# Performance work log

Hardware: AMD Instinct MI355X
Metric: run time of the kernel (lower is better)

Reference implementation:

```python
import jax, jax.numpy as jnp
import numpy as np

N = 100000
E = 1600000
IN = 256
H = 4
C = 64


def setup_inputs() -> dict:
    key = jax.random.key(0)
    k1, k2, k3, k4, k5, k6 = jax.random.split(key, 6)
    x = jax.random.normal(k1, (N, IN), dtype=jnp.float32)
    edge_index = jax.random.randint(k2, (2, E), 0, N, dtype=jnp.int64)
    W = jax.random.normal(k3, (IN, H * C), dtype=jnp.float32) * (1.0 / np.sqrt(IN))
    att_src = jax.random.normal(k4, (H, C), dtype=jnp.float32) * 0.1
    att_dst = jax.random.normal(k5, (H, C), dtype=jnp.float32) * 0.1
    bias = jax.random.normal(k6, (H * C,), dtype=jnp.float32) * 0.01
    return {"x": x, "edge_index": edge_index, "W": W, "att_src": att_src, "att_dst": att_dst, "bias": bias}


def reference(x, edge_index, W, att_src, att_dst, bias):
    n = x.shape[0]
    # PyG GATConv default: add self-loops
    loops = jnp.arange(n, dtype=edge_index.dtype)
    src = jnp.concatenate([edge_index[0], loops])  # [E+N]
    dst = jnp.concatenate([edge_index[1], loops])  # [E+N]
    xp = (x @ W).reshape(n, H, C)                   # [N,H,C]
    a_src = jnp.einsum('nhc,hc->nh', xp, att_src)   # [N,H]
    a_dst = jnp.einsum('nhc,hc->nh', xp, att_dst)   # [N,H]
    # per-edge attention logits, LeakyReLU(0.2)
    alpha = jax.nn.leaky_relu(a_src[src] + a_dst[dst], negative_slope=0.2)  # [E+N,H]
    # segment softmax over destination neighborhoods (every node has a self-loop)
    amax = jax.ops.segment_max(alpha, dst, num_segments=n)
    amax = jnp.where(jnp.isfinite(amax), amax, 0.0)
    ex = jnp.exp(alpha - amax[dst])
    denom = jax.ops.segment_sum(ex, dst, num_segments=n)
    w = ex / denom[dst]                              # [E+N,H]
    # weighted scatter-add of source features
    msg = xp[src] * w[..., None]                     # [E+N,H,C]
    agg = jax.ops.segment_sum(msg, dst, num_segments=n)  # [N,H,C]
    out = agg.reshape(n, H * C) + bias
    return jax.nn.elu(out)
```

## Files before the change

kernel.cpp:

```cpp
#include <hip/hip_runtime.h>
#include <hip/hip_fp16.h>

#define FDIM 256
#define NH 4

typedef float f32x4 __attribute__((ext_vector_type(4)));
typedef int   i32x4 __attribute__((ext_vector_type(4)));
typedef short short8v __attribute__((ext_vector_type(8)));
typedef unsigned short ushort_t;
typedef unsigned short ushort8 __attribute__((ext_vector_type(8)));

__device__ __forceinline__ float leaky02(float v) { return v > 0.0f ? v : 0.2f * v; }

__device__ __forceinline__ ushort_t f2bf(float f) {
    union { float f; unsigned int u; } v; v.f = f;
    unsigned int u = v.u + 0x7FFFu + ((v.u >> 16) & 1u);
    return (ushort_t)(u >> 16);
}

__device__ __forceinline__ float bf2f(ushort_t u) {
    union { float f; unsigned int u; } v;
    v.u = ((unsigned int)u) << 16;
    return v.f;
}

__device__ __forceinline__ void gload_lds16(const void* g, void* lds) {
    __builtin_amdgcn_global_load_lds((const __attribute__((address_space(1))) unsigned int*)g,
                                     (__attribute__((address_space(3))) unsigned int*)lds, 16, 0, 0);
}

__device__ __forceinline__ float recw(const i32x4& r, int h) {
    unsigned v = (h < 2) ? (unsigned)r.y : (unsigned)r.z;
    unsigned bits = (h & 1) ? (v >> 16) : (v & 0xFFFFu);
    __half_raw hr; hr.x = (unsigned short)bits;
    return __half2float(*reinterpret_cast<__half*>(&hr));
}

__global__ __launch_bounds__(256) void wprep_kernel(const float* __restrict__ W,
                                                    ushort_t* __restrict__ Wbf) {
    const int k = blockIdx.x;
    const int col = threadIdx.x;
    Wbf[(((size_t)(k >> 3) * 256 + col) << 3) + (k & 7)] = f2bf(W[(size_t)k * 256 + col]);
}

__global__ __launch_bounds__(512) void gemm_xp_kernel(const float* __restrict__ x,
                                                      const ushort_t* __restrict__ Wbf,
                                                      const float* __restrict__ att_s,
                                                      const float* __restrict__ att_d,
                                                      ushort_t* __restrict__ xpb,
                                                      float* __restrict__ a_src,
                                                      float* __restrict__ a_dst, int n,
                                                      const int* __restrict__ dst,
                                                      int* __restrict__ counts,
                                                      ushort_t* __restrict__ rank, int E) {
    __shared__ ushort_t a_lds[4096];
    __shared__ ushort_t b_lds[8192];
    const int t = threadIdx.x;

    const int w = t >> 6, l = t & 63;
    const int wm = w >> 2, wn = w & 3;
    const int row0 = blockIdx.x << 7;
    const int fr = l & 15, fk = l >> 4;

    const int arow = t & 127, akb = t >> 7;
    int grow = row0 + arow;
    if (grow >= n) grow = n - 1;
    const float* aptr = x + (size_t)grow * FDIM + (akb << 3);

    f32x4 acc[4][4] = {};

    for (int s = 0; s < 8; ++s) {
        float4 v0 = *(const float4*)(aptr + s * 32);
        float4 v1 = *(const float4*)(aptr + s * 32 + 4);
        ushort8 u;
        u[0]=f2bf(v0.x); u[1]=f2bf(v0.y); u[2]=f2bf(v0.z); u[3]=f2bf(v0.w);
        u[4]=f2bf(v1.x); u[5]=f2bf(v1.y); u[6]=f2bf(v1.z); u[7]=f2bf(v1.w);

        if (s) __syncthreads();

        *(ushort8*)&a_lds[(((size_t)akb << 7) + arow) << 3] = u;
        gload_lds16(Wbf + (size_t)s * 8192 + ((size_t)t << 3), (char*)b_lds + (w << 10));
        gload_lds16(Wbf + (size_t)s * 8192 + ((size_t)(t + 512) << 3), (char*)b_lds + 8192 + (w << 10));
        __syncthreads();

        short8v af[4], bfv[4];
        #pragma unroll
        for (int m = 0; m < 4; ++m)
            af[m] = *(const short8v*)&a_lds[(((size_t)fk << 7) + wm * 64 + m * 16 + fr) << 3];
        #pragma unroll
        for (int nf = 0; nf < 4; ++nf)
            bfv[nf] = *(const short8v*)&b_lds[(((size_t)fk << 8) + wn * 64 + nf * 16 + fr) << 3];
        #pragma unroll
        for (int m = 0; m < 4; ++m)
            #pragma unroll
            for (int nf = 0; nf < 4; ++nf)
                acc[m][nf] = __builtin_amdgcn_mfma_f32_16x16x32_bf16(af[m], bfv[nf], acc[m][nf], 0, 0, 0);
    }

    #pragma unroll
    for (int m = 0; m < 4; ++m) {
        const int r_ = row0 + wm * 64 + m * 16 + fk * 4;
        #pragma unroll
        for (int nf = 0; nf < 4; ++nf) {
            const int c_ = wn * 64 + nf * 16 + fr;
            #pragma unroll
            for (int j = 0; j < 4; ++j)
                if (r_ + j < n)
                    xpb[(size_t)(r_ + j) * FDIM + c_] = f2bf(acc[m][nf][j]);
        }
    }

    float att_sv[4], att_dv[4];
    #pragma unroll
    for (int nf = 0; nf < 4; ++nf) {
        att_sv[nf] = att_s[(wn << 6) + (nf << 4) + fr];
        att_dv[nf] = att_d[(wn << 6) + (nf << 4) + fr];
    }
    #pragma unroll
    for (int m = 0; m < 4; ++m) {
        #pragma unroll
        for (int j = 0; j < 4; ++j) {
            float ps = acc[m][0][j] * att_sv[0] + acc[m][1][j] * att_sv[1]
                     + acc[m][2][j] * att_sv[2] + acc[m][3][j] * att_sv[3];
            float pd = acc[m][0][j] * att_dv[0] + acc[m][1][j] * att_dv[1]
                     + acc[m][2][j] * att_dv[2] + acc[m][3][j] * att_dv[3];
            ps += __shfl_xor(ps, 1, 64); pd += __shfl_xor(pd, 1, 64);
            ps += __shfl_xor(ps, 2, 64); pd += __shfl_xor(pd, 2, 64);
            ps += __shfl_xor(ps, 4, 64); pd += __shfl_xor(pd, 4, 64);
            ps += __shfl_xor(ps, 8, 64); pd += __shfl_xor(pd, 8, 64);
            if (fr == 0) {
                const int r_ = row0 + wm * 64 + m * 16 + fk * 4 + j;
                if (r_ < n) {
                    a_src[r_ * NH + wn] = ps;
                    a_dst[r_ * NH + wn] = pd;
                }
            }
        }
    }

    {
        const int per = (E + gridDim.x - 1) / gridDim.x;
        const int lo = blockIdx.x * per;
        const int hi = min(lo + per, E);
        for (int e = lo + t; e < hi; e += 512) {
            const int d = __builtin_nontemporal_load(&dst[e]);
            rank[e] = (ushort_t)atomicAdd(&counts[d], 1);
        }
    }
}

__global__ __launch_bounds__(256) void scan_partial_kernel(const int* __restrict__ counts,
                                                           int* __restrict__ blockSums, int n) {
    __shared__ int sdata[256];
    const int b = blockIdx.x, t = threadIdx.x;
    const int base = b * 1024 + t * 4;
    int s = 0;
    #pragma unroll
    for (int j = 0; j < 4; ++j)
        if (base + j < n) s += counts[base + j];
    sdata[t] = s;
    __syncthreads();
    for (int off = 128; off > 0; off >>= 1) {
        if (t < off) sdata[t] += sdata[t + off];
        __syncthreads();
    }
    if (t == 0) blockSums[b] = sdata[0];
}

__global__ __launch_bounds__(256) void scan_final_kernel(const int* __restrict__ counts,
                                                         const int* __restrict__ blockSums,
                                                         int* __restrict__ offsets, int n, int nb) {
    __shared__ int s[256];
    __shared__ int bs[256];
    const int b = blockIdx.x, t = threadIdx.x;
    int bv = (t < nb) ? blockSums[t] : 0;
    bs[t] = bv;
    __syncthreads();
    for (int d = 1; d < 256; d <<= 1) {
        int u = (t >= d) ? bs[t - d] : 0;
        __syncthreads();
        bs[t] += u;
        __syncthreads();
    }
    const int blockOff = (b > 0) ? bs[b - 1] : 0;

    const int base = b * 1024 + t * 4;
    int c[4];
    int tsum = 0;
    #pragma unroll
    for (int j = 0; j < 4; ++j) {
        c[j] = (base + j < n) ? counts[base + j] : 0;
        tsum += c[j];
    }
    s[t] = tsum;
    __syncthreads();
    for (int d = 1; d < 256; d <<= 1) {
        int u = (t >= d) ? s[t - d] : 0;
        __syncthreads();
        s[t] += u;
        __syncthreads();
    }
    int run = s[t] - tsum + blockOff;
    #pragma unroll
    for (int j = 0; j < 4; ++j) {
        if (base + j < n) {
            offsets[base + j] = run;
            run += c[j];
        }
    }
}

__global__ void scatter_kernel(const int* __restrict__ src, const int* __restrict__ dst,
                               const ushort_t* __restrict__ rank,
                               const float* __restrict__ a_src, const float* __restrict__ a_dst,
                               const int* __restrict__ offsets,
                               i32x4* __restrict__ erec, int E) {
    int stride = gridDim.x * blockDim.x;
    for (int e = blockIdx.x * blockDim.x + threadIdx.x; e < E; e += stride) {
        const int s = __builtin_nontemporal_load(&src[e]);
        const int d = __builtin_nontemporal_load(&dst[e]);
        const int r = rank[e];
        const float4 as = ((const float4*)a_src)[s];
        const float4 ad = ((const float4*)a_dst)[d];
        const float w0 = __expf(leaky02(as.x + ad.x));
        const float w1 = __expf(leaky02(as.y + ad.y));
        const float w2 = __expf(leaky02(as.z + ad.z));
        const float w3 = __expf(leaky02(as.w + ad.w));
        union { __half2 h; int i; } p01, p23;
        p01.h = __floats2half2_rn(w0, w1);
        p23.h = __floats2half2_rn(w2, w3);
        i32x4 rec;
        rec.x = s; rec.y = p01.i; rec.z = p23.i; rec.w = 0;
        const int pos = offsets[d] + r;
        __builtin_nontemporal_store(rec, &erec[pos]);
    }
}

__global__ __launch_bounds__(256) void aggregate_kernel(const ushort_t* __restrict__ xpb,
                                                        const float* __restrict__ a_src,
                                                        const float* __restrict__ a_dst,
                                                        const int* __restrict__ offsets,
                                                        const int* __restrict__ counts,
                                                        const i32x4* __restrict__ erec,
                                                        const float* __restrict__ bias,
                                                        float* __restrict__ out, int n) {
    const int i = (blockIdx.x << 2) + (threadIdx.x >> 6);
    if (i >= n) return;
    const int lane = threadIdx.x & 63;
    const int halfid = lane >> 5, sl = lane & 31;
    const int h = sl >> 3;
    const size_t colb = (size_t)sl << 3;
    const int start = offsets[i];
    const int cnt = counts[i];
    const i32x4* recs = erec + start;

    float acc[8] = {};
    float den = 0.f;

    int e = 0;
    for (; e + 4 <= cnt; e += 4) {
        const i32x4 ra = recs[e + halfid];
        const i32x4 rb = recs[e + 2 + halfid];
        const ushort8 ua = *(const ushort8*)(xpb + (size_t)ra.x * FDIM + colb);
        const ushort8 ub = *(const ushort8*)(xpb + (size_t)rb.x * FDIM + colb);
        const float wa = recw(ra, h), wb = recw(rb, h);
        den += wa + wb;
        #pragma unroll
        for (int j = 0; j < 8; ++j) acc[j] = fmaf(wa, bf2f(ua[j]), acc[j]);
        #pragma unroll
        for (int j = 0; j < 8; ++j) acc[j] = fmaf(wb, bf2f(ub[j]), acc[j]);
    }
    for (; e < cnt; e += 2) {
        const int idx = e + halfid;
        const int cidx = idx < cnt ? idx : cnt - 1;
        const i32x4 r = recs[cidx];
        const ushort8 u = *(const ushort8*)(xpb + (size_t)r.x * FDIM + colb);
        const float wv = idx < cnt ? recw(r, h) : 0.f;
        den += wv;
        #pragma unroll
        for (int j = 0; j < 8; ++j) acc[j] = fmaf(wv, bf2f(u[j]), acc[j]);
    }
    if (halfid == 0) {
        const float ws = __expf(leaky02(a_src[i * NH + h] + a_dst[i * NH + h]));
        const ushort8 u = *(const ushort8*)(xpb + (size_t)i * FDIM + colb);
        den += ws;
        #pragma unroll
        for (int j = 0; j < 8; ++j) acc[j] = fmaf(ws, bf2f(u[j]), acc[j]);
    }
    den += __shfl_xor(den, 32, 64);
    #pragma unroll
    for (int j = 0; j < 8; ++j) acc[j] += __shfl_xor(acc[j], 32, 64);

    const float inv = 1.0f / den;
    const int c0 = (sl << 3) + (halfid << 2);
    const float4 b4 = *(const float4*)(bias + c0);
    const int jb = halfid << 2;
    f32x4 v;
    v.x = acc[jb + 0] * inv + b4.x;
    v.y = acc[jb + 1] * inv + b4.y;
    v.z = acc[jb + 2] * inv + b4.z;
    v.w = acc[jb + 3] * inv + b4.w;
    v.x = v.x > 0.f ? v.x : (__expf(v.x) - 1.f);
    v.y = v.y > 0.f ? v.y : (__expf(v.y) - 1.f);
    v.z = v.z > 0.f ? v.z : (__expf(v.z) - 1.f);
    v.w = v.w > 0.f ? v.w : (__expf(v.w) - 1.f);
    *(f32x4*)(out + (size_t)i * FDIM + c0) = v;
}

extern "C" void kernel_launch(void* const* d_in, const int* in_sizes, int n_in,
                              void* d_out, int out_size, void* d_ws, size_t ws_size,
                              hipStream_t stream) {
    const float* x       = (const float*)d_in[0];
    const int*   ei      = (const int*)d_in[1];
    const float* W       = (const float*)d_in[2];
    const float* att_s   = (const float*)d_in[3];
    const float* att_d   = (const float*)d_in[4];
    const float* bias    = (const float*)d_in[5];
    float* out = (float*)d_out;

    const int n = in_sizes[0] / FDIM;
    const int E = in_sizes[1] / 2;
    const int* src = ei;
    const int* dst = ei + E;

    char* ws = (char*)d_ws;
    size_t off = 0;
    auto alloc = [&](size_t bytes) -> void* {
        void* p = ws + off;
        off = (off + bytes + 255) & ~(size_t)255;
        return p;
    };
    ushort_t* xpb  = (ushort_t*)alloc((size_t)n * FDIM * sizeof(ushort_t));
    float* a_src   = (float*)alloc((size_t)n * NH * sizeof(float));
    float* a_dst   = (float*)alloc((size_t)n * NH * sizeof(float));
    int* counts    = (int*)alloc((size_t)n * sizeof(int));
    int* offsets   = (int*)alloc((size_t)n * sizeof(int));
    int* blockSums = (int*)alloc(256 * sizeof(int));
    ushort_t* rank = (ushort_t*)alloc((size_t)E * sizeof(ushort_t));
    i32x4* erec    = (i32x4*)alloc((size_t)E * sizeof(i32x4));
    ushort_t* Wbf  = (ushort_t*)alloc((size_t)FDIM * FDIM * sizeof(ushort_t));
    (void)ws_size;

    hipMemsetAsync(counts, 0, (size_t)n * sizeof(int), stream);

    wprep_kernel<<<256, 256, 0, stream>>>(W, Wbf);
    gemm_xp_kernel<<<(n + 127) / 128, 512, 0, stream>>>(x, Wbf, att_s, att_d, xpb, a_src, a_dst, n,
                                                        dst, counts, rank, E);
    const int nb = (n + 1023) / 1024;
    scan_partial_kernel<<<nb, 256, 0, stream>>>(counts, blockSums, n);
    scan_final_kernel<<<nb, 256, 0, stream>>>(counts, blockSums, offsets, n, nb);
    scatter_kernel<<<2048, 256, 0, stream>>>(src, dst, rank, a_src, a_dst, offsets, erec, E);
    aggregate_kernel<<<(n + 3) / 4, 256, 0, stream>>>(xpb, a_src, a_dst, offsets, counts, erec,
                                                      bias, out, n);
}
```

Baseline: 334.3 us.

## Pre-convert x to bf16 in separate kernel and load GEMM tiles via global_load_lds

Moves the fp32-to-bf16 conversion of x and the edge rank counting into a new prep kernel that writes a bf16 copy of x. The GEMM then streams both A and B tiles directly into LDS with global_load_lds instead of loading fp32 through registers, converting, and storing to LDS. This is meant to shorten the GEMM's per-stage latency and decouple the atomic counting from it. The cost is an extra full write and read of a 51 MB bf16 copy of x plus one more kernel launch.

New measurement: 332.1 us. Within noise of the previous version (-0.7%).

```diff
diff --git a/kernel.cpp b/kernel.cpp
--- a/kernel.cpp
+++ b/kernel.cpp
@@ -43,44 +43,70 @@
     Wbf[(((size_t)(k >> 3) * 256 + col) << 3) + (k & 7)] = f2bf(W[(size_t)k * 256 + col]);
 }
 
-__global__ __launch_bounds__(512) void gemm_xp_kernel(const float* __restrict__ x,
+__global__ __launch_bounds__(256) void xprep_kernel(const float* __restrict__ x,
+                                                    ushort_t* __restrict__ xb, int n,
+                                                    const int* __restrict__ dst,
+                                                    int* __restrict__ counts,
+                                                    ushort_t* __restrict__ rank, int E) {
+    const int stride = gridDim.x * blockDim.x;
+    const int gid = blockIdx.x * blockDim.x + threadIdx.x;
+    const int total8 = n * 32;
+    for (int idx = gid; idx < total8; idx += stride) {
+        const float4 v0 = ((const float4*)x)[(size_t)idx * 2];
+        const float4 v1 = ((const float4*)x)[(size_t)idx * 2 + 1];
+        ushort8 u;
+        u[0]=f2bf(v0.x); u[1]=f2bf(v0.y); u[2]=f2bf(v0.z); u[3]=f2bf(v0.w);
+        u[4]=f2bf(v1.x); u[5]=f2bf(v1.y); u[6]=f2bf(v1.z); u[7]=f2bf(v1.w);
+        *(ushort8*)(xb + (size_t)idx * 8) = u;
+    }
+    for (int e = gid; e < E; e += stride) {
+        const int d = __builtin_nontemporal_load(&dst[e]);
+        rank[e] = (ushort_t)atomicAdd(&counts[d], 1);
+    }
+}
+
+__global__ __launch_bounds__(512) void gemm_xp_kernel(const ushort_t* __restrict__ xb,
                                                       const ushort_t* __restrict__ Wbf,
                                                       const float* __restrict__ att_s,
                                                       const float* __restrict__ att_d,
                                                       ushort_t* __restrict__ xpb,
                                                       float* __restrict__ a_src,
-                                                      float* __restrict__ a_dst, int n,
-                                                      const int* __restrict__ dst,
-                                                      int* __restrict__ counts,
-                                                      ushort_t* __restrict__ rank, int E) {
+                                                      float* __restrict__ a_dst, int n) {
     __shared__ ushort_t a_lds[4096];
     __shared__ ushort_t b_lds[8192];
     const int t = threadIdx.x;
-
     const int w = t >> 6, l = t & 63;
     const int wm = w >> 2, wn = w & 3;
     const int row0 = blockIdx.x << 7;
     const int fr = l & 15, fk = l >> 4;
 
-    const int arow = t & 127, akb = t >> 7;
-    int grow = row0 + arow;
-    if (grow >= n) grow = n - 1;
-    const float* aptr = x + (size_t)grow * FDIM + (akb << 3);
+    const ushort_t* ptrA[2];
+    #pragma unroll
+    for (int rh = 0; rh < 2; ++rh) {
+        int r = row0 + rh * 64 + l;
+        if (r >= n) r = n - 1;
+        ptrA[rh] = xb + (size_t)r * FDIM;
+    }
+    const ushort_t* ptrB = Wbf + ((size_t)l << 3);
 
     f32x4 acc[4][4] = {};
 
     for (int s = 0; s < 8; ++s) {
-        float4 v0 = *(const float4*)(aptr + s * 32);
-        float4 v1 = *(const float4*)(aptr + s * 32 + 4);
-        ushort8 u;
-        u[0]=f2bf(v0.x); u[1]=f2bf(v0.y); u[2]=f2bf(v0.z); u[3]=f2bf(v0.w);
-        u[4]=f2bf(v1.x); u[5]=f2bf(v1.y); u[6]=f2bf(v1.z); u[7]=f2bf(v1.w);
-
         if (s) __syncthreads();
-
-        *(ushort8*)&a_lds[(((size_t)akb << 7) + arow) << 3] = u;
-        gload_lds16(Wbf + (size_t)s * 8192 + ((size_t)t << 3), (char*)b_lds + (w << 10));
-        gload_lds16(Wbf + (size_t)s * 8192 + ((size_t)(t + 512) << 3), (char*)b_lds + 8192 + (w << 10));
+        #pragma unroll
+        for (int j = 0; j < 3; ++j) {
+            const int c = w * 3 + j;
+            if (c < 8) {
+                const int kb = c >> 1, rh = c & 1;
+                gload_lds16(ptrA[rh] + s * 32 + kb * 8,
+                            (char*)a_lds + ((kb * 128 + rh * 64) << 4));
+            } else {
+                const int cc = c - 8;
+                const int kb = cc >> 2, q = cc & 3;
+                gload_lds16(ptrB + (((size_t)(s * 4 + kb) << 8) + q * 64) * 8,
+                            (char*)b_lds + ((kb * 256 + q * 64) << 4));
+            }
+        }
         __syncthreads();
 
         short8v af[4], bfv[4];
@@ -135,16 +161,6 @@
                     a_dst[r_ * NH + wn] = pd;
                 }
             }
-        }
-    }
-
-    {
-        const int per = (E + gridDim.x - 1) / gridDim.x;
-        const int lo = blockIdx.x * per;
-        const int hi = min(lo + per, E);
-        for (int e = lo + t; e < hi; e += 512) {
-            const int d = __builtin_nontemporal_load(&dst[e]);
-            rank[e] = (ushort_t)atomicAdd(&counts[d], 1);
         }
     }
 }
@@ -331,6 +347,7 @@
         return p;
     };
     ushort_t* xpb  = (ushort_t*)alloc((size_t)n * FDIM * sizeof(ushort_t));
+    ushort_t* xb   = (ushort_t*)alloc((size_t)n * FDIM * sizeof(ushort_t));
     float* a_src   = (float*)alloc((size_t)n * NH * sizeof(float));
     float* a_dst   = (float*)alloc((size_t)n * NH * sizeof(float));
     int* counts    = (int*)alloc((size_t)n * sizeof(int));
@@ -344,8 +361,8 @@
     hipMemsetAsync(counts, 0, (size_t)n * sizeof(int), stream);
 
     wprep_kernel<<<256, 256, 0, stream>>>(W, Wbf);
-    gemm_xp_kernel<<<(n + 127) / 128, 512, 0, stream>>>(x, Wbf, att_s, att_d, xpb, a_src, a_dst, n,
-                                                        dst, counts, rank, E);
+    xprep_kernel<<<2048, 256, 0, stream>>>(x, xb, n, dst, counts, rank, E);
+    gemm_xp_kernel<<<(n + 127) / 128, 512, 0, stream>>>(xb, Wbf, att_s, att_d, xpb, a_src, a_dst, n);
     const int nb = (n + 1023) / 1024;
     scan_partial_kernel<<<nb, 256, 0, stream>>>(counts, blockSums, n);
     scan_final_kernel<<<nb, 256, 0, stream>>>(counts, blockSums, offsets, n, nb);
```
